# Performance work log

Measured on AMD Instinct MI355X. Metric: run time of the kernel, lower is better.

## Reference

```python
import jax, jax.numpy as jnp
import numpy as np

T = 2048
C = 2048
N_HEAD = 16
HEAD_DIM = C // N_HEAD


def setup_inputs() -> dict:
    key = jax.random.key(0)
    k1, k2, k3 = jax.random.split(key, 3)
    x = jax.random.normal(k1, (T, C), dtype=jnp.float32)
    # eqx.nn.Linear weight convention: (out_features, in_features)
    W_attn = jax.random.normal(k2, (3 * C, C), dtype=jnp.float32) * (1.0 / np.sqrt(C))
    W_proj = jax.random.normal(k3, (C, C), dtype=jnp.float32) * (1.0 / np.sqrt(C))
    return {"x": x, "W_attn": W_attn, "W_proj": W_proj}


def reference(x, W_attn, W_proj):
    # qkv projection: (T, 3C)
    qkv = x @ W_attn.T
    q, k, v = jnp.split(qkv, 3, axis=-1)
    # reshape to (H, T, d)
    q = q.reshape(T, N_HEAD, HEAD_DIM).transpose(1, 0, 2)
    k = k.reshape(T, N_HEAD, HEAD_DIM).transpose(1, 0, 2)
    v = v.reshape(T, N_HEAD, HEAD_DIM).transpose(1, 0, 2)
    # scaled causal attention: (H, T, T)
    att = jnp.einsum('htd,hsd->hts', q, k)
    causal_mask = jnp.triu(jnp.ones((T, T), dtype=bool), k=1)  # mask future keys
    att = jnp.where(causal_mask, -jnp.inf, att)
    att = jax.nn.softmax(att / jnp.sqrt(jnp.float32(HEAD_DIM)), axis=-1)
    # attention output: (H, T, d) -> (T, C)
    out = jnp.einsum('hts,hsd->htd', att, v)
    out = out.transpose(1, 0, 2).reshape(T, C)
    return out @ W_proj.T
```

## Files before the change

### kernel.cpp

```cpp
#include <hip/hip_runtime.h>
#include <cstdint>

using bx8 = __attribute__((ext_vector_type(8))) __bf16;
using us8 = __attribute__((ext_vector_type(8))) unsigned short;
using fl8 = __attribute__((ext_vector_type(8))) float;
using fx4 = __attribute__((ext_vector_type(4))) float;

static __device__ inline unsigned short f2bf(float f) {
  unsigned u = __builtin_bit_cast(unsigned, f);
  unsigned r = 0x7FFFu + ((u >> 16) & 1u);
  return (unsigned short)((u + r) >> 16);
}
static __device__ inline float bf2f(unsigned short s) {
  return __builtin_bit_cast(float, (unsigned)s << 16);
}

static __device__ inline fx4 mfma16(bx8 a, bx8 b, fx4 c) {
  return __builtin_amdgcn_mfma_f32_16x16x32_bf16(a, b, c, 0, 0, 0);
}

#define DPP_ROR(x, k) __builtin_bit_cast(float, __builtin_amdgcn_update_dpp( \
    __builtin_bit_cast(int, x), __builtin_bit_cast(int, x), 0x120 | (k), 0xF, 0xF, false))

static __device__ inline float rowmax16(float v) {
  v = fmaxf(v, DPP_ROR(v, 1));
  v = fmaxf(v, DPP_ROR(v, 2));
  v = fmaxf(v, DPP_ROR(v, 4));
  v = fmaxf(v, DPP_ROR(v, 8));
  return v;
}
static __device__ inline float rowsum16(float v) {
  v += DPP_ROR(v, 1);
  v += DPP_ROR(v, 2);
  v += DPP_ROR(v, 4);
  v += DPP_ROR(v, 8);
  return v;
}

template <typename T> struct RegOf { using type = us8; };
template <> struct RegOf<float>  { using type = fl8; };

template <typename T>
static __device__ inline typename RegOf<T>::type load8(const T* p) {
  return *reinterpret_cast<const typename RegOf<T>::type*>(p);
}
static __device__ inline us8 toBf(us8 v) { return v; }
static __device__ inline us8 toBf(fl8 f) {
  us8 o;
#pragma unroll
  for (int j = 0; j < 8; ++j) {
    __bf16 b = (__bf16)f[j];
    o[j] = __builtin_bit_cast(unsigned short, b);
  }
  return o;
}

template <typename TA, typename TB, bool F32OUT>
__global__ __launch_bounds__(256) void gemm_bt(const TA* __restrict__ A,
                                               const TB* __restrict__ B,
                                               void* __restrict__ Cp,
                                               int M, int N, int K) {
  __shared__ alignas(16) unsigned short As[128 * 64];
  __shared__ alignas(16) unsigned short Bs[128 * 64];
  const int tid = threadIdx.x;
  const int w = tid >> 6, l = tid & 63;
  const int l16 = l & 15, lg = l >> 4;
  const int wr = w >> 1, wc = w & 1;
  const long mb = (long)blockIdx.y * 128, nb = (long)blockIdx.x * 128;

  const fx4 fz = {0.f, 0.f, 0.f, 0.f};
  fx4 acc[4][4];
#pragma unroll
  for (int i = 0; i < 4; ++i)
#pragma unroll
    for (int j = 0; j < 4; ++j) acc[i][j] = fz;

  const int sr  = tid >> 3;
  const int sc8 = (tid & 7) * 8;
  const int wbc = sc8 * 2;

  typename RegOf<TA>::type rA[4];
  typename RegOf<TB>::type rB[4];

#pragma unroll
  for (int p = 0; p < 4; ++p) {
    const int row = p * 32 + sr;
    rA[p] = load8(A + (mb + row) * (long)K + sc8);
    rB[p] = load8(B + (nb + row) * (long)K + sc8);
  }

  for (int k0 = 0; k0 < K; k0 += 64) {
    __syncthreads();
#pragma unroll
    for (int p = 0; p < 4; ++p) {
      const int row = p * 32 + sr;
      const int eo = row * 64 + ((wbc ^ ((row & 7) << 4)) >> 1);
      *reinterpret_cast<us8*>(&As[eo]) = toBf(rA[p]);
      *reinterpret_cast<us8*>(&Bs[eo]) = toBf(rB[p]);
    }
    if (k0 + 64 < K) {
#pragma unroll
      for (int p = 0; p < 4; ++p) {
        const int row = p * 32 + sr;
        rA[p] = load8(A + (mb + row) * (long)K + k0 + 64 + sc8);
        rB[p] = load8(B + (nb + row) * (long)K + k0 + 64 + sc8);
      }
    }
    __syncthreads();
#pragma unroll
    for (int kk = 0; kk < 2; ++kk) {
      bx8 a[4], b[4];
#pragma unroll
      for (int mf = 0; mf < 4; ++mf) {
        const int ra = wr * 64 + mf * 16 + l16;
        const int bc = kk * 64 + lg * 16;
        a[mf] = *reinterpret_cast<const bx8*>(&As[ra * 64 + ((bc ^ ((ra & 7) << 4)) >> 1)]);
      }
#pragma unroll
      for (int nf = 0; nf < 4; ++nf) {
        const int rb_ = wc * 64 + nf * 16 + l16;
        const int bc = kk * 64 + lg * 16;
        b[nf] = *reinterpret_cast<const bx8*>(&Bs[rb_ * 64 + ((bc ^ ((rb_ & 7) << 4)) >> 1)]);
      }
#pragma unroll
      for (int mf = 0; mf < 4; ++mf)
#pragma unroll
        for (int nf = 0; nf < 4; ++nf)
          acc[mf][nf] = mfma16(a[mf], b[nf], acc[mf][nf]);
    }
  }

#pragma unroll
  for (int mf = 0; mf < 4; ++mf)
#pragma unroll
    for (int nf = 0; nf < 4; ++nf)
#pragma unroll
      for (int r = 0; r < 4; ++r) {
        const long row = mb + wr * 64 + mf * 16 + lg * 4 + r;
        const long col = nb + wc * 64 + nf * 16 + l16;
        if (F32OUT)
          ((float*)Cp)[row * N + col] = acc[mf][nf][r];
        else
          ((unsigned short*)Cp)[row * N + col] = f2bf(acc[mf][nf][r]);
      }
}

__global__ __launch_bounds__(256) void fa_kernel(const unsigned short* __restrict__ qkv,
                                                 unsigned short* __restrict__ out,
                                                 unsigned short* __restrict__ Obuf,
                                                 float* __restrict__ ML) {
  __shared__ alignas(16) unsigned short Ks[64 * 136];
  __shared__ alignas(16) unsigned short Vt[128 * 72];
  __shared__ alignas(16) unsigned short Ps[4][16 * 72];

  const int id = blockIdx.x;
  int h, qt, t0, t1;
  bool partial;
  if (id < 512) {
    const int p = id >> 1, c = id & 1;
    qt = 31 - (p >> 4); h = p & 15;
    const int nt0 = (qt + 2) >> 1;
    t0 = c ? nt0 : 0;
    t1 = c ? (qt + 1) : nt0;
    partial = true;
  } else {
    const int s = id - 512;
    qt = 15 - (s >> 4); h = s & 15;
    t0 = 0; t1 = qt + 1;
    partial = false;
  }
  const int qb = qt * 64;

  const int tid = threadIdx.x;
  const int w = tid >> 6, l = tid & 63;
  const int l16 = l & 15, lg = l >> 4;
  const fx4 fz = {0.f, 0.f, 0.f, 0.f};

  const int kr = tid >> 4, kc8 = (tid & 15) * 8;
  const int kv = tid & 63, d0v = (tid >> 6) * 32;

  bx8 qf[4];
  {
    const long qrow = qb + w * 16 + l16;
    const unsigned short* qp = qkv + qrow * 6144L + h * 128 + lg * 8;
#pragma unroll
    for (int kc = 0; kc < 4; ++kc)
      qf[kc] = *reinterpret_cast<const bx8*>(qp + kc * 32);
  }

  fx4 o_acc[8];
#pragma unroll
  for (int i = 0; i < 8; ++i) o_acc[i] = fz;
  float m_r[4] = {-3e38f, -3e38f, -3e38f, -3e38f};
  float l_r[4] = {0.f, 0.f, 0.f, 0.f};

  us8 rK[4], rV[4];
  {
    const long kvb = (long)t0 * 64;
#pragma unroll
    for (int p = 0; p < 4; ++p)
      rK[p] = *reinterpret_cast<const us8*>(qkv + (kvb + p * 16 + kr) * 6144L + 2048 + h * 128 + kc8);
#pragma unroll
    for (int i = 0; i < 4; ++i)
      rV[i] = *reinterpret_cast<const us8*>(qkv + (kvb + kv) * 6144L + 4096 + h * 128 + d0v + i * 8);
  }

  for (int t = t0; t < t1; ++t) {
    __syncthreads();

#pragma unroll
    for (int p = 0; p < 4; ++p)
      *reinterpret_cast<us8*>(&Ks[(p * 16 + kr) * 136 + kc8]) = rK[p];
#pragma unroll
    for (int i = 0; i < 4; ++i)
#pragma unroll
      for (int j = 0; j < 8; ++j)
        Vt[(d0v + i * 8 + j) * 72 + kv] = rV[i][j];

    if (t + 1 < t1) {
      const long kvb = (long)(t + 1) * 64;
#pragma unroll
      for (int p = 0; p < 4; ++p)
        rK[p] = *reinterpret_cast<const us8*>(qkv + (kvb + p * 16 + kr) * 6144L + 2048 + h * 128 + kc8);
#pragma unroll
      for (int i = 0; i < 4; ++i)
        rV[i] = *reinterpret_cast<const us8*>(qkv + (kvb + kv) * 6144L + 4096 + h * 128 + d0v + i * 8);
    }
    __syncthreads();

    fx4 s[4];
#pragma unroll
    for (int nf = 0; nf < 4; ++nf) s[nf] = fz;
#pragma unroll
    for (int kc = 0; kc < 4; ++kc) {
#pragma unroll
      for (int nf = 0; nf < 4; ++nf) {
        const int rl = nf * 16 + l16;
        bx8 kb = *reinterpret_cast<const bx8*>(&Ks[rl * 136 + kc * 32 + lg * 8]);
        s[nf] = mfma16(qf[kc], kb, s[nf]);
      }
    }

    if (t == qt) {
#pragma unroll
      for (int nf = 0; nf < 4; ++nf) {
        const int kv_abs = t * 64 + nf * 16 + l16;
#pragma unroll
        for (int r = 0; r < 4; ++r) {
          const int q_abs = qb + w * 16 + lg * 4 + r;
          if (kv_abs > q_abs) s[nf][r] = -3e38f;
        }
      }
    }

    const float sc2 = 0.1275173831f;
    float pv[4][4];
#pragma unroll
    for (int r = 0; r < 4; ++r) {
      float rm = fmaxf(fmaxf(s[0][r], s[1][r]), fmaxf(s[2][r], s[3][r]));
      rm = rowmax16(rm);
      const float mn = fmaxf(m_r[r], rm);
      const float fac = exp2f((m_r[r] - mn) * sc2);
      m_r[r] = mn;
      float rs = 0.f;
#pragma unroll
      for (int nf = 0; nf < 4; ++nf) {
        const float p = exp2f((s[nf][r] - mn) * sc2);
        pv[nf][r] = p;
        rs += p;
      }
      rs = rowsum16(rs);
      l_r[r] = l_r[r] * fac + rs;
#pragma unroll
      for (int nf = 0; nf < 8; ++nf) o_acc[nf][r] *= fac;
    }

    unsigned short* psw = &Ps[w][0];
#pragma unroll
    for (int nf = 0; nf < 4; ++nf)
#pragma unroll
      for (int r = 0; r < 4; ++r)
        psw[(lg * 4 + r) * 72 + nf * 16 + l16] = f2bf(pv[nf][r]);

    bx8 pa[2];
#pragma unroll
    for (int kc = 0; kc < 2; ++kc)
      pa[kc] = *reinterpret_cast<const bx8*>(&psw[l16 * 72 + kc * 32 + lg * 8]);

#pragma unroll
    for (int nf = 0; nf < 8; ++nf) {
#pragma unroll
      for (int kc = 0; kc < 2; ++kc) {
        bx8 vb = *reinterpret_cast<const bx8*>(&Vt[(nf * 16 + l16) * 72 + kc * 32 + lg * 8]);
        o_acc[nf] = mfma16(pa[kc], vb, o_acc[nf]);
      }
    }
  }

  if (!partial) {
#pragma unroll
    for (int nf = 0; nf < 8; ++nf)
#pragma unroll
      for (int r = 0; r < 4; ++r) {
        const long row = qb + w * 16 + lg * 4 + r;
        const long col = h * 128 + nf * 16 + l16;
        out[row * 2048 + col] = f2bf(o_acc[nf][r] / l_r[r]);
      }
  } else {
    unsigned short* ob = Obuf + (long)id * 8192;
#pragma unroll
    for (int nf = 0; nf < 8; ++nf)
#pragma unroll
      for (int r = 0; r < 4; ++r) {
        const int row = w * 16 + lg * 4 + r;
        ob[row * 128 + nf * 16 + l16] = f2bf(o_acc[nf][r]);
      }
    if (l16 == 0) {
#pragma unroll
      for (int r = 0; r < 4; ++r) {
        const int row = w * 16 + lg * 4 + r;
        ML[((long)id * 64 + row) * 2 + 0] = m_r[r];
        ML[((long)id * 64 + row) * 2 + 1] = l_r[r];
      }
    }
  }
}

__global__ __launch_bounds__(256) void fa_combine(const unsigned short* __restrict__ Obuf,
                                                  const float* __restrict__ ML,
                                                  unsigned short* __restrict__ out) {
  const int p = blockIdx.x;
  const int qt = 31 - (p >> 4), h = p & 15;
  const int tid = threadIdx.x;
  const int row = tid >> 2;
  const int c0 = (tid & 3) * 32;

  const long idA = 2 * p, idB = 2 * p + 1;
  const float mA = ML[(idA * 64 + row) * 2 + 0];
  const float lA = ML[(idA * 64 + row) * 2 + 1];
  const float mB = ML[(idB * 64 + row) * 2 + 0];
  const float lB = ML[(idB * 64 + row) * 2 + 1];
  const float sc2 = 0.1275173831f;
  const float m = fmaxf(mA, mB);
  const float fA = exp2f((mA - m) * sc2);
  const float fB = exp2f((mB - m) * sc2);
  const float inv = 1.0f / (lA * fA + lB * fB);
  const float cA = fA * inv, cB = fB * inv;

  const unsigned short* oa = Obuf + idA * 8192 + row * 128 + c0;
  const unsigned short* obp = Obuf + idB * 8192 + row * 128 + c0;
  unsigned short* dst = out + (long)(qt * 64 + row) * 2048 + h * 128 + c0;
#pragma unroll
  for (int j = 0; j < 4; ++j) {
    us8 a = *reinterpret_cast<const us8*>(oa + j * 8);
    us8 b = *reinterpret_cast<const us8*>(obp + j * 8);
    ushort4 o0, o1;
    float v0, v1, v2, v3;
    v0 = bf2f(a[0]) * cA + bf2f(b[0]) * cB;
    v1 = bf2f(a[1]) * cA + bf2f(b[1]) * cB;
    v2 = bf2f(a[2]) * cA + bf2f(b[2]) * cB;
    v3 = bf2f(a[3]) * cA + bf2f(b[3]) * cB;
    o0 = {f2bf(v0), f2bf(v1), f2bf(v2), f2bf(v3)};
    v0 = bf2f(a[4]) * cA + bf2f(b[4]) * cB;
    v1 = bf2f(a[5]) * cA + bf2f(b[5]) * cB;
    v2 = bf2f(a[6]) * cA + bf2f(b[6]) * cB;
    v3 = bf2f(a[7]) * cA + bf2f(b[7]) * cB;
    o1 = {f2bf(v0), f2bf(v1), f2bf(v2), f2bf(v3)};
    *reinterpret_cast<ushort4*>(dst + j * 8) = o0;
    *reinterpret_cast<ushort4*>(dst + j * 8 + 4) = o1;
  }
}

extern "C" void kernel_launch(void* const* d_in, const int* in_sizes, int n_in,
                              void* d_out, int out_size, void* d_ws, size_t ws_size,
                              hipStream_t stream) {
  const float* x  = (const float*)d_in[0];
  const float* Wa = (const float*)d_in[1];
  const float* Wp = (const float*)d_in[2];
  float* out = (float*)d_out;
  char* ws = (char*)d_ws;

  unsigned short* qkvb  = (unsigned short*)(ws);
  unsigned short* Obuf  = (unsigned short*)(ws + (24ull << 20));
  float*          ML    = (float*)(ws + (32ull << 20));
  unsigned short* attnb = (unsigned short*)(ws + (33ull << 20));

  gemm_bt<float, float, false><<<dim3(48, 16), 256, 0, stream>>>(x, Wa, (void*)qkvb, 2048, 6144, 2048);

  fa_kernel<<<768, 256, 0, stream>>>(qkvb, attnb, Obuf, ML);

  fa_combine<<<256, 256, 0, stream>>>(Obuf, ML, attnb);

  gemm_bt<unsigned short, float, true><<<dim3(16, 16), 256, 0, stream>>>(attnb, Wp, (void*)out, 2048, 2048, 2048);
}
```

Baseline: 183.5 us.

## Pre-convert QKV GEMM inputs to bf16 and use 256x256 direct-to-LDS pipelined GEMM

Adds a conversion kernel that turns x and W_attn into bf16 buffers, then runs the QKV projection with a new 256x256-tile, 512-thread GEMM. The GEMM loads global data straight into swizzled LDS through global_load_lds, with a four-stage buffer ring and vmcnt-based waits. The aim is more data reuse per tile and less conversion and register-staging cost inside the GEMM loop. In exchange it adds two extra passes over memory to convert about 16M floats each call, and it reuses workspace regions, which requires the buffer lifetimes not to overlap. The 192-block grid may also underfill the GPU's CUs.

Result: no change. 180.0 us (-1.9%).

```diff
diff --git a/kernel.cpp b/kernel.cpp
--- a/kernel.cpp
+++ b/kernel.cpp
@@ -17,6 +17,19 @@
 
 static __device__ inline fx4 mfma16(bx8 a, bx8 b, fx4 c) {
   return __builtin_amdgcn_mfma_f32_16x16x32_bf16(a, b, c, 0, 0, 0);
+}
+
+static __device__ inline void gload16(const void* g, void* lds) {
+  __builtin_amdgcn_global_load_lds(
+      (const __attribute__((address_space(1))) void*)g,
+      (__attribute__((address_space(3))) void*)lds,
+      16, 0, 0);
+}
+#define VMCNT(n) asm volatile("s_waitcnt vmcnt(" #n ")" ::: "memory")
+static __device__ inline void wave_barrier() {
+  __builtin_amdgcn_sched_barrier(0);
+  __builtin_amdgcn_s_barrier();
+  __builtin_amdgcn_sched_barrier(0);
 }
 
 #define DPP_ROR(x, k) __builtin_bit_cast(float, __builtin_amdgcn_update_dpp( \
@@ -35,6 +48,102 @@
   v += DPP_ROR(v, 4);
   v += DPP_ROR(v, 8);
   return v;
+}
+
+__global__ __launch_bounds__(256) void f2b_kernel(const float* __restrict__ in,
+                                                  unsigned short* __restrict__ out,
+                                                  int n) {
+  int i = (blockIdx.x * 256 + threadIdx.x) * 4;
+  if (i >= n) return;
+  float4 v = *reinterpret_cast<const float4*>(in + i);
+  ushort4 o;
+  o.x = f2bf(v.x); o.y = f2bf(v.y); o.z = f2bf(v.z); o.w = f2bf(v.w);
+  *reinterpret_cast<ushort4*>(out + i) = o;
+}
+
+__global__ __launch_bounds__(512, 2) void gemm256(const unsigned short* __restrict__ A,
+                                                  const unsigned short* __restrict__ B,
+                                                  unsigned short* __restrict__ C,
+                                                  int M, int N, int K) {
+  __shared__ unsigned short lds[4][2][256 * 32];
+
+  const int tid = threadIdx.x;
+  const int w = tid >> 6, l = tid & 63;
+  const int l16 = l & 15, lg = l >> 4;
+  const int wr = w >> 2, wc = w & 3;
+  const long mb = (long)blockIdx.y * 256, nb = (long)blockIdx.x * 256;
+
+  const int lr = l >> 2;
+  const int sw = (((l & 3) ^ (lr & 3)) * 8);
+  const unsigned short* Ag = A + (mb + w * 32 + lr) * (long)K + sw;
+  const unsigned short* Bg = B + (nb + w * 32 + lr) * (long)K + sw;
+
+  const int rdcol = ((lg ^ (l16 & 3)) * 16);
+
+  const fx4 fz = {0.f, 0.f, 0.f, 0.f};
+  fx4 acc[8][4];
+#pragma unroll
+  for (int i = 0; i < 8; ++i)
+#pragma unroll
+    for (int j = 0; j < 4; ++j) acc[i][j] = fz;
+
+  const int nt = K >> 5;
+
+  auto stage = [&](int tp) {
+    const int db = tp & 3;
+    const unsigned short* as = Ag + tp * 32;
+    const unsigned short* bs = Bg + tp * 32;
+    char* al = (char*)&lds[db][0][0] + w * 32 * 64;
+    char* bl = (char*)&lds[db][1][0] + w * 32 * 64;
+    gload16(as, al);
+    gload16(as + 16 * (long)K, al + 1024);
+    gload16(bs, bl);
+    gload16(bs + 16 * (long)K, bl + 1024);
+  };
+
+  auto compute = [&](int bt) {
+    const char* Ab = (const char*)&lds[bt][0][0] + (wr * 128 + l16) * 64 + rdcol;
+    const char* Bb = (const char*)&lds[bt][1][0] + (wc * 64 + l16) * 64 + rdcol;
+    bx8 bf[4];
+#pragma unroll
+    for (int nf = 0; nf < 4; ++nf)
+      bf[nf] = *reinterpret_cast<const bx8*>(Bb + nf * 1024);
+    __builtin_amdgcn_s_setprio(1);
+#pragma unroll
+    for (int mf = 0; mf < 8; ++mf) {
+      bx8 av = *reinterpret_cast<const bx8*>(Ab + mf * 1024);
+#pragma unroll
+      for (int nf = 0; nf < 4; ++nf)
+        acc[mf][nf] = mfma16(av, bf[nf], acc[mf][nf]);
+    }
+    __builtin_amdgcn_s_setprio(0);
+  };
+
+  stage(0); stage(1); stage(2);
+  VMCNT(8);
+  wave_barrier();
+
+  int t = 0;
+  for (; t < nt - 3; ++t) {
+    stage(t + 3);
+    compute(t & 3);
+    VMCNT(8);
+    wave_barrier();
+  }
+  compute(t & 3); VMCNT(4); wave_barrier(); ++t;
+  compute(t & 3); VMCNT(0); wave_barrier(); ++t;
+  compute(t & 3);
+
+#pragma unroll
+  for (int mf = 0; mf < 8; ++mf)
+#pragma unroll
+    for (int nf = 0; nf < 4; ++nf)
+#pragma unroll
+      for (int r = 0; r < 4; ++r) {
+        const long row = mb + wr * 128 + mf * 16 + lg * 4 + r;
+        const long col = nb + wc * 64 + nf * 16 + l16;
+        C[row * N + col] = f2bf(acc[mf][nf][r]);
+      }
 }
 
 template <typename T> struct RegOf { using type = us8; };
@@ -380,12 +489,17 @@
   float* out = (float*)d_out;
   char* ws = (char*)d_ws;
 
-  unsigned short* qkvb  = (unsigned short*)(ws);
-  unsigned short* Obuf  = (unsigned short*)(ws + (24ull << 20));
-  float*          ML    = (float*)(ws + (32ull << 20));
-  unsigned short* attnb = (unsigned short*)(ws + (33ull << 20));
-
-  gemm_bt<float, float, false><<<dim3(48, 16), 256, 0, stream>>>(x, Wa, (void*)qkvb, 2048, 6144, 2048);
+  unsigned short* wab   = (unsigned short*)(ws);
+  unsigned short* qkvb  = (unsigned short*)(ws + (24ull << 20));
+  unsigned short* xb    = (unsigned short*)(ws + (48ull << 20));
+  unsigned short* Obuf  = (unsigned short*)(ws);
+  float*          ML    = (float*)(ws + (8ull << 20));
+  unsigned short* attnb = (unsigned short*)(ws + (48ull << 20));
+
+  f2b_kernel<<<4096, 256, 0, stream>>>(x, xb, 2048 * 2048);
+  f2b_kernel<<<12288, 256, 0, stream>>>(Wa, wab, 6144 * 2048);
+
+  gemm256<<<dim3(24, 8), 512, 0, stream>>>(xb, wab, qkvb, 2048, 6144, 2048);
 
   fa_kernel<<<768, 256, 0, stream>>>(qkvb, attnb, Obuf, ML);
 
```
